# Kernel optimization log

Measured on AMD Instinct MI355X. Metric: run time of the kernel, lower is better.

Reference implementation:

```python
import jax, jax.numpy as jnp
import numpy as np

NUM_USERS = 100000
NUM_SERVICES = 50000
EMB_DIM = 32
CONTEXT = 3
NUM_EDGES = 1600000
BATCH = 2048


def gcn_conv(x, W, b, src, dst, n):
    """PyG-style GCNConv: add self-loops, symmetric D^-1/2 (A+I) D^-1/2 norm,
    linear transform then aggregate, plus bias."""
    h = x @ W  # [n, d_out]
    loops = jnp.arange(n, dtype=src.dtype)
    s = jnp.concatenate([src, loops])  # message sources
    d = jnp.concatenate([dst, loops])  # aggregation targets
    ones = jnp.ones(s.shape[0], dtype=x.dtype)
    deg = jax.ops.segment_sum(ones, d, num_segments=n)  # in-degree incl. self-loop
    dis = jnp.where(deg > 0, jax.lax.rsqrt(jnp.maximum(deg, 1e-12)), 0.0)
    norm = dis[s] * dis[d]  # [E + n]
    msgs = h[s] * norm[:, None]
    out = jax.ops.segment_sum(msgs, d, num_segments=n)
    return out + b


def setup_inputs() -> dict:
    key = jax.random.key(0)
    ks = jax.random.split(key, 12)
    user_idx = jax.random.randint(ks[0], (BATCH,), 0, NUM_USERS)
    context_idx = jax.random.randint(ks[1], (BATCH, CONTEXT), 0, NUM_SERVICES)
    edge_index = jax.random.randint(ks[2], (2, NUM_EDGES), 0, NUM_SERVICES)
    s = 1.0 / np.sqrt(EMB_DIM)
    user_emb = jax.random.normal(ks[3], (NUM_USERS, EMB_DIM), jnp.float32)
    service_emb = jax.random.normal(ks[4], (NUM_SERVICES, EMB_DIM), jnp.float32)
    W1 = jax.random.normal(ks[5], (EMB_DIM, EMB_DIM), jnp.float32) * s
    b1 = jnp.zeros((EMB_DIM,), jnp.float32)
    W2 = jax.random.normal(ks[6], (EMB_DIM, EMB_DIM), jnp.float32) * s
    b2 = jnp.zeros((EMB_DIM,), jnp.float32)
    fin = EMB_DIM * (CONTEXT + 1)
    fc_W = jax.random.normal(ks[7], (fin, NUM_SERVICES), jnp.float32) / np.sqrt(fin)
    fc_b = jnp.zeros((NUM_SERVICES,), jnp.float32)
    return {"user_idx": user_idx, "context_idx": context_idx, "edge_index": edge_index,
            "user_emb": user_emb, "service_emb": service_emb,
            "W1": W1, "b1": b1, "W2": W2, "b2": b2, "fc_W": fc_W, "fc_b": fc_b}


def reference(user_idx, context_idx, edge_index, user_emb, service_emb,
              W1, b1, W2, b2, fc_W, fc_b):
    src, dst = edge_index[0], edge_index[1]
    user_vec = user_emb[user_idx]  # [B, d]
    g = jax.nn.relu(gcn_conv(service_emb, W1, b1, src, dst, NUM_SERVICES))
    g = gcn_conv(g, W2, b2, src, dst, NUM_SERVICES)  # [n, d]
    ctx = g[context_idx].reshape(context_idx.shape[0], -1)  # [B, C*d]
    x = jnp.concatenate([user_vec, ctx], axis=1)  # [B, (C+1)*d]
    return x @ fc_W + fc_b  # [B, num_services]
```

## Files before the change

### kernel.cpp

```cpp
#include <hip/hip_runtime.h>

#define N_SERVICES 50000
#define N_PAD      50048
#define N_EDGES    1600000
#define N_CTX      6144
#define EMB        32
#define BATCH      2048
#define FIN        128
#define N_TILES    782
#define BM         128
#define M_CHUNKS   16
#define N_CHAINS   64
#define GEMM_BLKS  (M_CHUNKS * N_CHAINS)
#define RUN_BASE   12
#define RUN_EXTRA  14

#define RANGE      8192
#define R_RANGES   7
#define C_CHUNKS   64
#define PSTR       50000
#define EPC        (N_EDGES / C_CHUNKS)
#define I4PC       (EPC / 4)

typedef __attribute__((ext_vector_type(4))) float f32x4;
typedef __attribute__((ext_vector_type(2))) float f32x2;
typedef __attribute__((ext_vector_type(8))) short short8;

__device__ inline unsigned short f2bf(float f) {
    unsigned u = __float_as_uint(f);
    unsigned r = (u + 0x7FFFu + ((u >> 16) & 1u)) >> 16;
    return (unsigned short)r;
}
__device__ inline float bf2f(unsigned short b) {
    return __uint_as_float(((unsigned)b) << 16);
}


__global__ __launch_bounds__(256) void k_tiled_count(const int* __restrict__ dst,
                                                     unsigned short* __restrict__ partial) {
    __shared__ int hist[RANGE];
    int t = threadIdx.x;
    int r = blockIdx.x / C_CHUNKS;
    int c = blockIdx.x % C_CHUNKS;
    for (int i = t; i < RANGE; i += 256) hist[i] = 0;
    __syncthreads();
    const int4* d4 = (const int4*)(dst + c * EPC);
    for (int i = t; i < I4PC; i += 256) {
        int4 d = d4[i];
        if ((d.x >> 13) == r) atomicAdd(&hist[d.x & (RANGE - 1)], 1);
        if ((d.y >> 13) == r) atomicAdd(&hist[d.y & (RANGE - 1)], 1);
        if ((d.z >> 13) == r) atomicAdd(&hist[d.z & (RANGE - 1)], 1);
        if ((d.w >> 13) == r) atomicAdd(&hist[d.w & (RANGE - 1)], 1);
    }
    __syncthreads();
    int base = r * RANGE;
    unsigned short* p = partial + (size_t)c * PSTR;
    for (int i = t; i < RANGE; i += 256) {
        int n = base + i;
        if (n < N_SERVICES) p[n] = (unsigned short)hist[i];
    }
}


__global__ void k_scan_block(const unsigned short* __restrict__ partial,
                             float* __restrict__ dis,
                             int* __restrict__ tmp, int* __restrict__ blocksum) {
    __shared__ int s[256];
    int t = threadIdx.x, i = blockIdx.x * 256 + t;
    int v = 0;
    if (i < N_SERVICES) {
#pragma unroll 8
        for (int c = 0; c < C_CHUNKS; ++c) v += partial[(size_t)c * PSTR + i];
        dis[i] = rsqrtf((float)(v + 1));
    }
    s[t] = v;
    __syncthreads();
#pragma unroll
    for (int o = 1; o < 256; o <<= 1) {
        int x = 0;
        if (t >= o) x = s[t - o];
        __syncthreads();
        if (t >= o) s[t] += x;
        __syncthreads();
    }
    if (i < N_SERVICES) tmp[i] = s[t] - v;
    if (t == 255) blocksum[blockIdx.x] = s[255];
}


__global__ __launch_bounds__(256) void k_scanfin_tf(
    const int* __restrict__ tmp, const int* __restrict__ blocksum,
    int* __restrict__ row_start,
    const int* __restrict__ ctx_idx, int* __restrict__ mask,
    int* __restrict__ ctx_list, int* __restrict__ ctx_count,
    unsigned short* __restrict__ partial,
    const float* __restrict__ in, const float* __restrict__ W1,
    const float* __restrict__ dis, unsigned short* __restrict__ h) {
    __shared__ int s[256];
    __shared__ float Ws[EMB][EMB + 1];
    __shared__ float rows[8][EMB];
    int t = threadIdx.x;

    if (blockIdx.x < 196) {
        int v = (t < 196) ? blocksum[t] : 0;
        s[t] = v;
        __syncthreads();
#pragma unroll
        for (int o = 1; o < 256; o <<= 1) {
            int x = 0;
            if (t >= o) x = s[t - o];
            __syncthreads();
            if (t >= o) s[t] += x;
            __syncthreads();
        }
        int prefix = (blockIdx.x == 0) ? 0 : s[blockIdx.x - 1];
        int i = blockIdx.x * 256 + t;
        if (i < N_SERVICES) {
            row_start[i] = tmp[i] + prefix;
            int acc = 0;
#pragma unroll 8
            for (int c = 0; c < C_CHUNKS; ++c) {
                size_t idx = (size_t)c * PSTR + i;
                int cnt = partial[idx];
                partial[idx] = (unsigned short)acc;
                acc += cnt;
            }
        }
        if (i < N_CTX) {
            int n = ctx_idx[i];
            if (atomicExch(&mask[n], 1) == 0)
                ctx_list[atomicAdd(ctx_count, 1)] = n;
        }
        if (i == 0) row_start[N_SERVICES] = N_EDGES;
    } else {
        int j = t & 31, li = t >> 5;
        for (int i = t; i < EMB * EMB; i += 256) Ws[i >> 5][i & 31] = W1[i];
        int node = (blockIdx.x - 196) * 8 + li;
        if (node < N_SERVICES) rows[li][j] = in[node * EMB + j];
        __syncthreads();
        if (node < N_SERVICES) {
            float acc = 0.f;
#pragma unroll
            for (int k = 0; k < EMB; ++k) acc = fmaf(rows[li][k], Ws[k][j], acc);
            h[node * EMB + j] = f2bf(acc * dis[node]);
        }
    }
}


__global__ __launch_bounds__(256) void k_fill(const int* __restrict__ src,
                                              const int* __restrict__ dst,
                                              const int* __restrict__ row_start,
                                              const unsigned short* __restrict__ partial,
                                              int* __restrict__ csr_src) {
    __shared__ int cur[RANGE];
    int t = threadIdx.x;
    int r = blockIdx.x / C_CHUNKS;
    int c = blockIdx.x % C_CHUNKS;
    int base = r * RANGE;
    const unsigned short* off = partial + (size_t)c * PSTR;
    for (int i = t; i < RANGE; i += 256) {
        int n = base + i;
        cur[i] = (n < N_SERVICES) ? (row_start[n] + off[n]) : 0;
    }
    __syncthreads();
    const int4* d4 = (const int4*)(dst + c * EPC);
    const int4* s4 = (const int4*)(src + c * EPC);
    for (int i = t; i < I4PC; i += 256) {
        int4 d = d4[i];
        int4 s = s4[i];
        if ((d.x >> 13) == r) csr_src[atomicAdd(&cur[d.x & (RANGE - 1)], 1)] = s.x;
        if ((d.y >> 13) == r) csr_src[atomicAdd(&cur[d.y & (RANGE - 1)], 1)] = s.y;
        if ((d.z >> 13) == r) csr_src[atomicAdd(&cur[d.z & (RANGE - 1)], 1)] = s.z;
        if ((d.w >> 13) == r) csr_src[atomicAdd(&cur[d.w & (RANGE - 1)], 1)] = s.w;
    }
}


__global__ __launch_bounds__(256) void k_agg_tf(
    const int* __restrict__ row_start, const int* __restrict__ csr_src,
    const float* __restrict__ dis, const unsigned int* __restrict__ h2,
    const float* __restrict__ b, const float* __restrict__ W2,
    unsigned short* __restrict__ hout) {
    __shared__ float gr[16][33];
    __shared__ float Ws[32][33];
    int t = threadIdx.x;
    for (int i = t; i < EMB * EMB; i += 256) Ws[i >> 5][i & 31] = W2[i];

    int j2 = t & 15;
    int local = t >> 4;
    int node = blockIdx.x * 16 + local;
    int e = row_start[node], e1 = row_start[node + 1];
    float al0 = 0.f, ah0 = 0.f, al1 = 0.f, ah1 = 0.f;
    float al2 = 0.f, ah2 = 0.f, al3 = 0.f, ah3 = 0.f;
    for (; e + 4 <= e1; e += 4) {
        int s0 = csr_src[e], s1 = csr_src[e + 1], s2 = csr_src[e + 2], s3 = csr_src[e + 3];
        unsigned v0 = h2[s0 * 16 + j2], v1 = h2[s1 * 16 + j2];
        unsigned v2 = h2[s2 * 16 + j2], v3 = h2[s3 * 16 + j2];
        al0 += bf2f((unsigned short)(v0 & 0xffff)); ah0 += bf2f((unsigned short)(v0 >> 16));
        al1 += bf2f((unsigned short)(v1 & 0xffff)); ah1 += bf2f((unsigned short)(v1 >> 16));
        al2 += bf2f((unsigned short)(v2 & 0xffff)); ah2 += bf2f((unsigned short)(v2 >> 16));
        al3 += bf2f((unsigned short)(v3 & 0xffff)); ah3 += bf2f((unsigned short)(v3 >> 16));
    }
    for (; e < e1; ++e) {
        unsigned v0 = h2[csr_src[e] * 16 + j2];
        al0 += bf2f((unsigned short)(v0 & 0xffff)); ah0 += bf2f((unsigned short)(v0 >> 16));
    }
    float dn = dis[node];
    unsigned vn = h2[node * 16 + j2];
    float lo = dn * ((al0 + al1) + (al2 + al3) + bf2f((unsigned short)(vn & 0xffff))) + b[j2 * 2];
    float hi = dn * ((ah0 + ah1) + (ah2 + ah3) + bf2f((unsigned short)(vn >> 16))) + b[j2 * 2 + 1];
    gr[local][j2 * 2]     = fmaxf(lo, 0.f);
    gr[local][j2 * 2 + 1] = fmaxf(hi, 0.f);
    __syncthreads();

    int d = t & 31;
    int l0 = t >> 5;
    float s0 = 0.f, s1 = 0.f;
#pragma unroll
    for (int k = 0; k < EMB; ++k) {
        float w = Ws[k][d];
        s0 = fmaf(gr[l0][k], w, s0);
        s1 = fmaf(gr[l0 + 8][k], w, s1);
    }
    int n0 = blockIdx.x * 16 + l0;
    hout[(size_t)n0 * EMB + d]       = f2bf(s0 * dis[n0]);
    hout[(size_t)(n0 + 8) * EMB + d] = f2bf(s1 * dis[n0 + 8]);
}


__global__ void k_agg_ctx(const int* __restrict__ row_start, const int* __restrict__ csr_src,
                          const float* __restrict__ dis, const unsigned int* __restrict__ h2,
                          const float* __restrict__ b, const int* __restrict__ ctx_list,
                          const int* __restrict__ ctx_count, float* __restrict__ out) {
    int t = threadIdx.x;
    int j2 = t & 15;
    int slot = blockIdx.x * 16 + (t >> 4);
    if (slot >= *ctx_count) return;
    int node = ctx_list[slot];
    int e = row_start[node], e1 = row_start[node + 1];
    float al0 = 0.f, ah0 = 0.f, al1 = 0.f, ah1 = 0.f;
    float al2 = 0.f, ah2 = 0.f, al3 = 0.f, ah3 = 0.f;
    for (; e + 4 <= e1; e += 4) {
        int s0 = csr_src[e], s1 = csr_src[e + 1], s2 = csr_src[e + 2], s3 = csr_src[e + 3];
        unsigned v0 = h2[s0 * 16 + j2], v1 = h2[s1 * 16 + j2];
        unsigned v2 = h2[s2 * 16 + j2], v3 = h2[s3 * 16 + j2];
        al0 += bf2f((unsigned short)(v0 & 0xffff)); ah0 += bf2f((unsigned short)(v0 >> 16));
        al1 += bf2f((unsigned short)(v1 & 0xffff)); ah1 += bf2f((unsigned short)(v1 >> 16));
        al2 += bf2f((unsigned short)(v2 & 0xffff)); ah2 += bf2f((unsigned short)(v2 >> 16));
        al3 += bf2f((unsigned short)(v3 & 0xffff)); ah3 += bf2f((unsigned short)(v3 >> 16));
    }
    for (; e < e1; ++e) {
        unsigned v0 = h2[csr_src[e] * 16 + j2];
        al0 += bf2f((unsigned short)(v0 & 0xffff)); ah0 += bf2f((unsigned short)(v0 >> 16));
    }
    float dn = dis[node];
    unsigned vn = h2[node * 16 + j2];
    float lo = dn * ((al0 + al1) + (al2 + al3) + bf2f((unsigned short)(vn & 0xffff))) + b[j2 * 2];
    float hi = dn * ((ah0 + ah1) + (ah2 + ah3) + bf2f((unsigned short)(vn >> 16))) + b[j2 * 2 + 1];
    f32x2 o; o.x = lo; o.y = hi;
    *(f32x2*)&out[node * EMB + j2 * 2] = o;
}


__global__ void k_gather(const int* __restrict__ user_idx, const int* __restrict__ ctx_idx,
                         const float* __restrict__ user_emb, const float* __restrict__ g2,
                         unsigned short* __restrict__ x) {
    int t = blockIdx.x * 256 + threadIdx.x;
    int b = t >> 7, p = t & 127;
    float v;
    if (p < EMB) {
        v = user_emb[user_idx[b] * EMB + p];
    } else {
        int c = (p - EMB) >> 5, j = p & 31;
        v = g2[ctx_idx[b * 3 + c] * EMB + j];
    }
    x[t] = f2bf(v);
}


__global__ __launch_bounds__(256) void k_cvtW(const float* __restrict__ W,
                                              short* __restrict__ Wt,
                                              int* __restrict__ mask,
                                              int* __restrict__ ctx_count) {
    int gid = blockIdx.x * 256 + threadIdx.x;
    if (gid < N_SERVICES) mask[gid] = 0;
    if (gid == 0) *ctx_count = 0;

    __shared__ short lds[128][33];
    int t = threadIdx.x;
    int n0 = blockIdx.x * 32;
    int nx = t & 31;
    int n  = n0 + nx;
    int kg = t >> 5;
#pragma unroll
    for (int r = 0; r < 16; ++r) {
        int k = r * 8 + kg;
        float v = (n < N_SERVICES) ? W[k * N_SERVICES + n] : 0.f;
        lds[k][nx] = (short)f2bf(v);
    }
    __syncthreads();
    int nr = t >> 3;
    int kc = (t & 7) * 16;
    short tmp[16];
#pragma unroll
    for (int i = 0; i < 16; ++i) tmp[i] = lds[kc + i][nr];
    short8* dstp = (short8*)(Wt + (size_t)(n0 + nr) * FIN + kc);
    dstp[0] = *(short8*)&tmp[0];
    dstp[1] = *(short8*)&tmp[8];
}


__global__ __launch_bounds__(256, 2) void k_gemm3(
    const short* __restrict__ A, const short* __restrict__ Bt,
    const float* __restrict__ bias, float* __restrict__ out) {
    __shared__ float tile[2][BM][68];
    int t = threadIdx.x;
    int w = t >> 6;
    int l = t & 63;
    int lr = l & 15;
    int lg = l >> 4;
    int mc = blockIdx.x >> 6;
    int c  = blockIdx.x & (N_CHAINS - 1);
    int nt0 = c * RUN_BASE + (c < RUN_EXTRA ? c : RUN_EXTRA);
    int cnt = RUN_BASE + (c < RUN_EXTRA ? 1 : 0);
    int m_base = mc * BM;

    short8 a[8][4];
#pragma unroll
    for (int mi = 0; mi < 8; ++mi) {
        const short* arow = A + (size_t)(m_base + mi * 16 + lr) * FIN + lg * 8;
#pragma unroll
        for (int ks = 0; ks < 4; ++ks) a[mi][ks] = *(const short8*)(arow + ks * 32);
    }

    const short* bbase = Bt + (size_t)(w * 16 + lr) * FIN + lg * 8;
    short8 b0[4], b1[4];
    {
        const short* p = bbase + (size_t)nt0 * 64 * FIN;
#pragma unroll
        for (int ks = 0; ks < 4; ++ks) b0[ks] = *(const short8*)(p + ks * 32);
    }

    int scol = lr * 4;
    int p = 0;

    for (int i = 0; i < cnt; ++i) {
        int nt = nt0 + i;
        if (i + 1 < cnt) {
            const short* pp = bbase + (size_t)(nt + 1) * 64 * FIN;
#pragma unroll
            for (int ks = 0; ks < 4; ++ks) b1[ks] = *(const short8*)(pp + ks * 32);
        }
#pragma unroll
        for (int mi = 0; mi < 8; ++mi) {
            f32x4 acc = {};
#pragma unroll
            for (int ks = 0; ks < 4; ++ks)
                acc = __builtin_amdgcn_mfma_f32_16x16x32_bf16(b0[ks], a[mi][ks], acc, 0, 0, 0);
            *(f32x4*)&tile[p][mi * 16 + lr][w * 16 + lg * 4] = acc;
        }
        __syncthreads();
        {
            int gcol = nt * 64 + scol;
            bool ok = gcol < N_SERVICES;
            f32x4 bv = {};
            if (ok) bv = *(const f32x4*)&bias[gcol];
            float* ob = out + (size_t)m_base * N_SERVICES + gcol;
#pragma unroll
            for (int si = 0; si < 8; ++si) {
                int row = w * 32 + si * 4 + lg;
                f32x4 v = *(const f32x4*)&tile[p][row][scol] + bv;
                if (ok)
                    __builtin_nontemporal_store(
                        v, (f32x4*)(ob + (size_t)row * N_SERVICES));
            }
        }
        p ^= 1;
#pragma unroll
        for (int ks = 0; ks < 4; ++ks) b0[ks] = b1[ks];
    }
}


extern "C" void kernel_launch(void* const* d_in, const int* in_sizes, int n_in,
                              void* d_out, int out_size, void* d_ws, size_t ws_size,
                              hipStream_t stream) {
    const int*   user_idx    = (const int*)d_in[0];
    const int*   ctx_idx     = (const int*)d_in[1];
    const int*   ei          = (const int*)d_in[2];
    const float* user_emb    = (const float*)d_in[3];
    const float* service_emb = (const float*)d_in[4];
    const float* W1          = (const float*)d_in[5];
    const float* b1          = (const float*)d_in[6];
    const float* W2          = (const float*)d_in[7];
    const float* b2          = (const float*)d_in[8];
    const float* fcW         = (const float*)d_in[9];
    const float* fcb         = (const float*)d_in[10];
    float* out = (float*)d_out;

    const int* src = ei;
    const int* dst = ei + N_EDGES;

    char* ws = (char*)d_ws;
    float*          dis       = (float*)(ws);
    unsigned short* h1        = (unsigned short*)(ws + 200000);
    unsigned short* h2b       = (unsigned short*)(ws + 3400000);
    float*          g         = (float*)(ws + 6600000);
    unsigned short* partial   = (unsigned short*)(ws + 6600000);
    unsigned short* xb        = (unsigned short*)(ws + 13000000);
    short*          Wt        = (short*)(ws + 13524288);
    int*            row_start = (int*)(ws + 26336576);
    int*            csr_src   = (int*)(ws + 26736580);
    int*            tmp       = (int*)(ws + 26736580);
    int*            blocksum  = (int*)(ws + 33136580);
    int*            mask      = (int*)(ws + 33137604);
    int*            ctx_list  = (int*)(ws + 33337604);
    int*            ctx_count = (int*)(ws + 33362180);

    k_cvtW<<<N_PAD / 32, 256, 0, stream>>>(fcW, Wt, mask, ctx_count);

    k_tiled_count<<<R_RANGES * C_CHUNKS, 256, 0, stream>>>(dst, partial);
    k_scan_block<<<196, 256, 0, stream>>>(partial, dis, tmp, blocksum);
    k_scanfin_tf<<<196 + 6250, 256, 0, stream>>>(tmp, blocksum, row_start,
                                                 ctx_idx, mask, ctx_list, ctx_count,
                                                 partial, service_emb, W1, dis, h1);
    k_fill<<<R_RANGES * C_CHUNKS, 256, 0, stream>>>(src, dst, row_start, partial, csr_src);

    k_agg_tf<<<3125, 256, 0, stream>>>(row_start, csr_src, dis,
                                       (const unsigned int*)h1, b1, W2, h2b);
    k_agg_ctx<<<N_CTX / 16, 256, 0, stream>>>(row_start, csr_src, dis,
                                              (const unsigned int*)h2b, b2,
                                              ctx_list, ctx_count, g);

    k_gather<<<BATCH * FIN / 256, 256, 0, stream>>>(user_idx, ctx_idx, user_emb, g, xb);

    k_gemm3<<<GEMM_BLKS, 256, 0, stream>>>((const short*)xb, Wt, fcb, out);
}
```

Baseline: 219.8 us.

## Merge weight conversion with degree count and fuse ctx aggregation into gather

Merges the fc weight transpose/bf16 conversion and the dst histogram into one launch with shared LDS. The last-layer aggregation now runs once per (batch, context) slot and writes bf16 straight into the GEMM input. This drops the dedup mask, ctx_list and the separate gather kernel, and removes two launches plus the fp32 g round-trip. In exchange, nodes that appear several times in context_idx get aggregated more than once instead of once.

```diff
diff --git a/kernel.cpp b/kernel.cpp
--- a/kernel.cpp
+++ b/kernel.cpp
@@ -21,6 +21,7 @@
 #define PSTR       50000
 #define EPC        (N_EDGES / C_CHUNKS)
 #define I4PC       (EPC / 4)
+#define CVT_BLKS   (N_PAD / 32)
 
 typedef __attribute__((ext_vector_type(4))) float f32x4;
 typedef __attribute__((ext_vector_type(2))) float f32x2;
@@ -36,28 +37,56 @@
 }
 
 
-__global__ __launch_bounds__(256) void k_tiled_count(const int* __restrict__ dst,
-                                                     unsigned short* __restrict__ partial) {
-    __shared__ int hist[RANGE];
-    int t = threadIdx.x;
-    int r = blockIdx.x / C_CHUNKS;
-    int c = blockIdx.x % C_CHUNKS;
-    for (int i = t; i < RANGE; i += 256) hist[i] = 0;
-    __syncthreads();
-    const int4* d4 = (const int4*)(dst + c * EPC);
-    for (int i = t; i < I4PC; i += 256) {
-        int4 d = d4[i];
-        if ((d.x >> 13) == r) atomicAdd(&hist[d.x & (RANGE - 1)], 1);
-        if ((d.y >> 13) == r) atomicAdd(&hist[d.y & (RANGE - 1)], 1);
-        if ((d.z >> 13) == r) atomicAdd(&hist[d.z & (RANGE - 1)], 1);
-        if ((d.w >> 13) == r) atomicAdd(&hist[d.w & (RANGE - 1)], 1);
-    }
-    __syncthreads();
-    int base = r * RANGE;
-    unsigned short* p = partial + (size_t)c * PSTR;
-    for (int i = t; i < RANGE; i += 256) {
-        int n = base + i;
-        if (n < N_SERVICES) p[n] = (unsigned short)hist[i];
+__global__ __launch_bounds__(256) void k_prep(const float* __restrict__ W,
+                                              short* __restrict__ Wt,
+                                              const int* __restrict__ dst,
+                                              unsigned short* __restrict__ partial) {
+    __shared__ __align__(16) char smem[32768];
+    int t = threadIdx.x;
+
+    if (blockIdx.x < CVT_BLKS) {
+        short (*lds)[33] = (short(*)[33])smem;
+        int n0 = blockIdx.x * 32;
+        int nx = t & 31;
+        int n  = n0 + nx;
+        int kg = t >> 5;
+#pragma unroll
+        for (int r = 0; r < 16; ++r) {
+            int k = r * 8 + kg;
+            float v = (n < N_SERVICES) ? W[k * N_SERVICES + n] : 0.f;
+            lds[k][nx] = (short)f2bf(v);
+        }
+        __syncthreads();
+        int nr = t >> 3;
+        int kc = (t & 7) * 16;
+        short tmpv[16];
+#pragma unroll
+        for (int i = 0; i < 16; ++i) tmpv[i] = lds[kc + i][nr];
+        short8* dstp = (short8*)(Wt + (size_t)(n0 + nr) * FIN + kc);
+        dstp[0] = *(short8*)&tmpv[0];
+        dstp[1] = *(short8*)&tmpv[8];
+    } else {
+        int* hist = (int*)smem;
+        int bid = blockIdx.x - CVT_BLKS;
+        int r = bid / C_CHUNKS;
+        int c = bid % C_CHUNKS;
+        for (int i = t; i < RANGE; i += 256) hist[i] = 0;
+        __syncthreads();
+        const int4* d4 = (const int4*)(dst + c * EPC);
+        for (int i = t; i < I4PC; i += 256) {
+            int4 d = d4[i];
+            if ((d.x >> 13) == r) atomicAdd(&hist[d.x & (RANGE - 1)], 1);
+            if ((d.y >> 13) == r) atomicAdd(&hist[d.y & (RANGE - 1)], 1);
+            if ((d.z >> 13) == r) atomicAdd(&hist[d.z & (RANGE - 1)], 1);
+            if ((d.w >> 13) == r) atomicAdd(&hist[d.w & (RANGE - 1)], 1);
+        }
+        __syncthreads();
+        int base = r * RANGE;
+        unsigned short* p = partial + (size_t)c * PSTR;
+        for (int i = t; i < RANGE; i += 256) {
+            int n = base + i;
+            if (n < N_SERVICES) p[n] = (unsigned short)hist[i];
+        }
     }
 }
 
@@ -91,8 +120,6 @@
 __global__ __launch_bounds__(256) void k_scanfin_tf(
     const int* __restrict__ tmp, const int* __restrict__ blocksum,
     int* __restrict__ row_start,
-    const int* __restrict__ ctx_idx, int* __restrict__ mask,
-    int* __restrict__ ctx_list, int* __restrict__ ctx_count,
     unsigned short* __restrict__ partial,
     const float* __restrict__ in, const float* __restrict__ W1,
     const float* __restrict__ dis, unsigned short* __restrict__ h) {
@@ -125,11 +152,6 @@
                 partial[idx] = (unsigned short)acc;
                 acc += cnt;
             }
-        }
-        if (i < N_CTX) {
-            int n = ctx_idx[i];
-            if (atomicExch(&mask[n], 1) == 0)
-                ctx_list[atomicAdd(ctx_count, 1)] = n;
         }
         if (i == 0) row_start[N_SERVICES] = N_EDGES;
     } else {
@@ -229,85 +251,50 @@
 }
 
 
-__global__ void k_agg_ctx(const int* __restrict__ row_start, const int* __restrict__ csr_src,
-                          const float* __restrict__ dis, const unsigned int* __restrict__ h2,
-                          const float* __restrict__ b, const int* __restrict__ ctx_list,
-                          const int* __restrict__ ctx_count, float* __restrict__ out) {
+__global__ void k_agg_gather(const int* __restrict__ row_start, const int* __restrict__ csr_src,
+                             const float* __restrict__ dis, const unsigned int* __restrict__ h2,
+                             const float* __restrict__ b,
+                             const int* __restrict__ user_idx, const int* __restrict__ ctx_idx,
+                             const float* __restrict__ user_emb,
+                             unsigned short* __restrict__ xb) {
     int t = threadIdx.x;
     int j2 = t & 15;
-    int slot = blockIdx.x * 16 + (t >> 4);
-    if (slot >= *ctx_count) return;
-    int node = ctx_list[slot];
-    int e = row_start[node], e1 = row_start[node + 1];
-    float al0 = 0.f, ah0 = 0.f, al1 = 0.f, ah1 = 0.f;
-    float al2 = 0.f, ah2 = 0.f, al3 = 0.f, ah3 = 0.f;
-    for (; e + 4 <= e1; e += 4) {
-        int s0 = csr_src[e], s1 = csr_src[e + 1], s2 = csr_src[e + 2], s3 = csr_src[e + 3];
-        unsigned v0 = h2[s0 * 16 + j2], v1 = h2[s1 * 16 + j2];
-        unsigned v2 = h2[s2 * 16 + j2], v3 = h2[s3 * 16 + j2];
-        al0 += bf2f((unsigned short)(v0 & 0xffff)); ah0 += bf2f((unsigned short)(v0 >> 16));
-        al1 += bf2f((unsigned short)(v1 & 0xffff)); ah1 += bf2f((unsigned short)(v1 >> 16));
-        al2 += bf2f((unsigned short)(v2 & 0xffff)); ah2 += bf2f((unsigned short)(v2 >> 16));
-        al3 += bf2f((unsigned short)(v3 & 0xffff)); ah3 += bf2f((unsigned short)(v3 >> 16));
-    }
-    for (; e < e1; ++e) {
-        unsigned v0 = h2[csr_src[e] * 16 + j2];
-        al0 += bf2f((unsigned short)(v0 & 0xffff)); ah0 += bf2f((unsigned short)(v0 >> 16));
-    }
-    float dn = dis[node];
-    unsigned vn = h2[node * 16 + j2];
-    float lo = dn * ((al0 + al1) + (al2 + al3) + bf2f((unsigned short)(vn & 0xffff))) + b[j2 * 2];
-    float hi = dn * ((ah0 + ah1) + (ah2 + ah3) + bf2f((unsigned short)(vn >> 16))) + b[j2 * 2 + 1];
-    f32x2 o; o.x = lo; o.y = hi;
-    *(f32x2*)&out[node * EMB + j2 * 2] = o;
-}
-
-
-__global__ void k_gather(const int* __restrict__ user_idx, const int* __restrict__ ctx_idx,
-                         const float* __restrict__ user_emb, const float* __restrict__ g2,
-                         unsigned short* __restrict__ x) {
-    int t = blockIdx.x * 256 + threadIdx.x;
-    int b = t >> 7, p = t & 127;
-    float v;
-    if (p < EMB) {
-        v = user_emb[user_idx[b] * EMB + p];
+    int u = blockIdx.x * 16 + (t >> 4);
+    if (u < N_CTX) {
+        int bb = u / 3, cc = u - bb * 3;
+        int node = ctx_idx[u];
+        int e = row_start[node], e1 = row_start[node + 1];
+        float al0 = 0.f, ah0 = 0.f, al1 = 0.f, ah1 = 0.f;
+        float al2 = 0.f, ah2 = 0.f, al3 = 0.f, ah3 = 0.f;
+        for (; e + 4 <= e1; e += 4) {
+            int s0 = csr_src[e], s1 = csr_src[e + 1], s2 = csr_src[e + 2], s3 = csr_src[e + 3];
+            unsigned v0 = h2[s0 * 16 + j2], v1 = h2[s1 * 16 + j2];
+            unsigned v2 = h2[s2 * 16 + j2], v3 = h2[s3 * 16 + j2];
+            al0 += bf2f((unsigned short)(v0 & 0xffff)); ah0 += bf2f((unsigned short)(v0 >> 16));
+            al1 += bf2f((unsigned short)(v1 & 0xffff)); ah1 += bf2f((unsigned short)(v1 >> 16));
+            al2 += bf2f((unsigned short)(v2 & 0xffff)); ah2 += bf2f((unsigned short)(v2 >> 16));
+            al3 += bf2f((unsigned short)(v3 & 0xffff)); ah3 += bf2f((unsigned short)(v3 >> 16));
+        }
+        for (; e < e1; ++e) {
+            unsigned v0 = h2[csr_src[e] * 16 + j2];
+            al0 += bf2f((unsigned short)(v0 & 0xffff)); ah0 += bf2f((unsigned short)(v0 >> 16));
+        }
+        float dn = dis[node];
+        unsigned vn = h2[node * 16 + j2];
+        float lo = dn * ((al0 + al1) + (al2 + al3) + bf2f((unsigned short)(vn & 0xffff))) + b[j2 * 2];
+        float hi = dn * ((ah0 + ah1) + (ah2 + ah3) + bf2f((unsigned short)(vn >> 16))) + b[j2 * 2 + 1];
+        ushort2 o;
+        o.x = f2bf(lo);
+        o.y = f2bf(hi);
+        *(ushort2*)&xb[(size_t)bb * FIN + EMB + cc * EMB + j2 * 2] = o;
     } else {
-        int c = (p - EMB) >> 5, j = p & 31;
-        v = g2[ctx_idx[b * 3 + c] * EMB + j];
-    }
-    x[t] = f2bf(v);
-}
-
-
-__global__ __launch_bounds__(256) void k_cvtW(const float* __restrict__ W,
-                                              short* __restrict__ Wt,
-                                              int* __restrict__ mask,
-                                              int* __restrict__ ctx_count) {
-    int gid = blockIdx.x * 256 + threadIdx.x;
-    if (gid < N_SERVICES) mask[gid] = 0;
-    if (gid == 0) *ctx_count = 0;
-
-    __shared__ short lds[128][33];
-    int t = threadIdx.x;
-    int n0 = blockIdx.x * 32;
-    int nx = t & 31;
-    int n  = n0 + nx;
-    int kg = t >> 5;
-#pragma unroll
-    for (int r = 0; r < 16; ++r) {
-        int k = r * 8 + kg;
-        float v = (n < N_SERVICES) ? W[k * N_SERVICES + n] : 0.f;
-        lds[k][nx] = (short)f2bf(v);
-    }
-    __syncthreads();
-    int nr = t >> 3;
-    int kc = (t & 7) * 16;
-    short tmp[16];
-#pragma unroll
-    for (int i = 0; i < 16; ++i) tmp[i] = lds[kc + i][nr];
-    short8* dstp = (short8*)(Wt + (size_t)(n0 + nr) * FIN + kc);
-    dstp[0] = *(short8*)&tmp[0];
-    dstp[1] = *(short8*)&tmp[8];
+        int bb = u - N_CTX;
+        f32x2 v = *(const f32x2*)&user_emb[(size_t)user_idx[bb] * EMB + j2 * 2];
+        ushort2 o;
+        o.x = f2bf(v.x);
+        o.y = f2bf(v.y);
+        *(ushort2*)&xb[(size_t)bb * FIN + j2 * 2] = o;
+    }
 }
 
 
@@ -406,7 +393,6 @@
     float*          dis       = (float*)(ws);
     unsigned short* h1        = (unsigned short*)(ws + 200000);
     unsigned short* h2b       = (unsigned short*)(ws + 3400000);
-    float*          g         = (float*)(ws + 6600000);
     unsigned short* partial   = (unsigned short*)(ws + 6600000);
     unsigned short* xb        = (unsigned short*)(ws + 13000000);
     short*          Wt        = (short*)(ws + 13524288);
@@ -414,26 +400,18 @@
     int*            csr_src   = (int*)(ws + 26736580);
     int*            tmp       = (int*)(ws + 26736580);
     int*            blocksum  = (int*)(ws + 33136580);
-    int*            mask      = (int*)(ws + 33137604);
-    int*            ctx_list  = (int*)(ws + 33337604);
-    int*            ctx_count = (int*)(ws + 33362180);
-
-    k_cvtW<<<N_PAD / 32, 256, 0, stream>>>(fcW, Wt, mask, ctx_count);
-
-    k_tiled_count<<<R_RANGES * C_CHUNKS, 256, 0, stream>>>(dst, partial);
+
+    k_prep<<<CVT_BLKS + R_RANGES * C_CHUNKS, 256, 0, stream>>>(fcW, Wt, dst, partial);
     k_scan_block<<<196, 256, 0, stream>>>(partial, dis, tmp, blocksum);
     k_scanfin_tf<<<196 + 6250, 256, 0, stream>>>(tmp, blocksum, row_start,
-                                                 ctx_idx, mask, ctx_list, ctx_count,
                                                  partial, service_emb, W1, dis, h1);
     k_fill<<<R_RANGES * C_CHUNKS, 256, 0, stream>>>(src, dst, row_start, partial, csr_src);
 
     k_agg_tf<<<3125, 256, 0, stream>>>(row_start, csr_src, dis,
                                        (const unsigned int*)h1, b1, W2, h2b);
-    k_agg_ctx<<<N_CTX / 16, 256, 0, stream>>>(row_start, csr_src, dis,
-                                              (const unsigned int*)h2b, b2,
-                                              ctx_list, ctx_count, g);
-
-    k_gather<<<BATCH * FIN / 256, 256, 0, stream>>>(user_idx, ctx_idx, user_emb, g, xb);
+    k_agg_gather<<<512, 256, 0, stream>>>(row_start, csr_src, dis,
+                                          (const unsigned int*)h2b, b2,
+                                          user_idx, ctx_idx, user_emb, xb);
 
     k_gemm3<<<GEMM_BLKS, 256, 0, stream>>>((const short*)xb, Wt, fcb, out);
 }
```

Result: faster. 214.9 us (-2.3%).
